# Kernel tuning notes

Hardware: AMD Instinct MI355X
Metric: run time of the kernel (lower is better)

Reference implementation:

```python
import jax, jax.numpy as jnp
import numpy as np

B, S, D_IN, D_OUT = 4, 2048, 4096, 4096
SPARSE_FRACTION = 0.9


def setup_inputs() -> dict:
    key = jax.random.key(0)
    k_x, k_w, k_m = jax.random.split(key, 3)
    x = jax.random.normal(k_x, (B, S, D_IN), dtype=jnp.float32)
    # kaiming_uniform_(a=sqrt(5)) -> U(-bound, bound), bound = sqrt(6/((1+a^2)*fan_in)) = 1/sqrt(fan_in)
    bound = 1.0 / np.sqrt(D_IN)
    weight = jax.random.uniform(k_w, (D_OUT, D_IN), dtype=jnp.float32,
                                minval=-bound, maxval=bound)
    # mask: exactly (1 - sparse_fraction) of entries are True (random permutation)
    num_params = D_OUT * D_IN
    num_sparse = int(num_params * SPARSE_FRACTION)
    perm = jax.random.permutation(k_m, num_params)
    mask_flat = jnp.ones((num_params,), dtype=jnp.float32).at[perm[:num_sparse]].set(0.0)
    mask = mask_flat.reshape(D_OUT, D_IN).astype(jnp.bool_)
    return {"x": x, "weight": weight, "mask": mask}


def reference(x, weight, mask):
    # masked_weight = weight * mask; out = x @ masked_weight.T
    masked_weight = weight * mask.astype(weight.dtype)  # [out, in]
    return jnp.einsum('bsi,oi->bso', x, masked_weight)
```

## Files before the change

### kernel.cpp

```cpp
#include <hip/hip_runtime.h>
#include <stdint.h>


static constexpr int Mdim = 8192;
static constexpr int Ndim = 4096;
static constexpr int Kdim = 4096;
static constexpr int BM = 128;
static constexpr int BN = 128;
static constexpr int BK = 64;

typedef __attribute__((ext_vector_type(8))) short short8;
typedef __attribute__((ext_vector_type(4))) float float4v;
typedef __attribute__((ext_vector_type(16))) float float16v;
typedef __attribute__((ext_vector_type(4))) int int4v;
typedef __attribute__((ext_vector_type(8))) unsigned short ushort8;

__device__ __forceinline__ unsigned short f32_to_bf16(float f) {
  union { float f; uint32_t u; } c; c.f = f;
  uint32_t u = c.u;
  u += 0x7fffu + ((u >> 16) & 1u);
  return (unsigned short)(u >> 16);
}

__global__ void detect_mask_kernel(const unsigned char* __restrict__ m, int* __restrict__ flag) {
  int found = 0;
  const int total = 1 << 20;
  for (int p = blockIdx.x * blockDim.x + threadIdx.x; p < total;
       p += gridDim.x * blockDim.x)
    found |= (m[4 * p + 1] != 0);
  if (__any(found) && (threadIdx.x & 63) == 0) atomicOr(flag, 1);
}

__global__ void cvt_x_kernel(const float* __restrict__ x, unsigned short* __restrict__ o) {
  long i = (blockIdx.x * (long)blockDim.x + threadIdx.x) * 8;
  float4v v0 = *(const float4v*)(x + i);
  float4v v1 = *(const float4v*)(x + i + 4);
  ushort8 r;
  r[0] = f32_to_bf16(v0[0]); r[1] = f32_to_bf16(v0[1]);
  r[2] = f32_to_bf16(v0[2]); r[3] = f32_to_bf16(v0[3]);
  r[4] = f32_to_bf16(v1[0]); r[5] = f32_to_bf16(v1[1]);
  r[6] = f32_to_bf16(v1[2]); r[7] = f32_to_bf16(v1[3]);
  *(ushort8*)(o + i) = r;
}

__global__ void cvt_w_kernel(const float* __restrict__ w, const unsigned char* __restrict__ mraw,
                             const int* __restrict__ flag, unsigned short* __restrict__ o) {
  long i = (blockIdx.x * (long)blockDim.x + threadIdx.x) * 8;
  float4v w0 = *(const float4v*)(w + i);
  float4v w1 = *(const float4v*)(w + i + 4);
  int m[8];
  if (*flag) {
    unsigned long long mb = *(const unsigned long long*)(mraw + i);
#pragma unroll
    for (int j = 0; j < 8; ++j) m[j] = ((mb >> (8 * j)) & 0xffull) != 0;
  } else {
    int4v a = *(const int4v*)((const int*)mraw + i);
    int4v b = *(const int4v*)((const int*)mraw + i + 4);
#pragma unroll
    for (int j = 0; j < 4; ++j) { m[j] = a[j] != 0; m[4 + j] = b[j] != 0; }
  }
  ushort8 r;
  r[0] = f32_to_bf16(m[0] ? w0[0] : 0.0f);
  r[1] = f32_to_bf16(m[1] ? w0[1] : 0.0f);
  r[2] = f32_to_bf16(m[2] ? w0[2] : 0.0f);
  r[3] = f32_to_bf16(m[3] ? w0[3] : 0.0f);
  r[4] = f32_to_bf16(m[4] ? w1[0] : 0.0f);
  r[5] = f32_to_bf16(m[5] ? w1[1] : 0.0f);
  r[6] = f32_to_bf16(m[6] ? w1[2] : 0.0f);
  r[7] = f32_to_bf16(m[7] ? w1[3] : 0.0f);
  *(ushort8*)(o + i) = r;
}

__global__ __launch_bounds__(256) void gemm_bt_kernel(const unsigned short* __restrict__ X,
                                                      const unsigned short* __restrict__ W,
                                                      float* __restrict__ O) {
  __shared__ short sA[BM * BK];
  __shared__ short sB[BN * BK];

  const int tid = threadIdx.x;
  const int lane = tid & 63;
  const int wave = tid >> 6;
  const int wr = wave >> 1;
  const int wc = wave & 1;

  const int bid = blockIdx.x;
  const int grp512 = bid >> 9;
  const int rres = bid & 511;
  const int tm = (grp512 << 4) | (rres & 15);
  const int tn = rres >> 4;
  const int row0 = tm * BM;
  const int col0 = tn * BN;

  float16v acc[2][2];
#pragma unroll
  for (int i = 0; i < 2; ++i)
#pragma unroll
    for (int j = 0; j < 2; ++j)
#pragma unroll
      for (int r = 0; r < 16; ++r) acc[i][j][r] = 0.f;

  int srow[4], scol[4];
#pragma unroll
  for (int r = 0; r < 4; ++r) {
    int c = r * 256 + tid;
    srow[r] = c >> 3;
    scol[r] = (((c & 7) ^ (srow[r] & 7)) * 8);
  }

  const int ml = lane & 31;
  const int kg = lane >> 5;
  const int sw = lane & 7;

  for (int kt = 0; kt < Kdim; kt += BK) {
#pragma unroll
    for (int r = 0; r < 4; ++r) {
      const unsigned short* gA = X + (long)(row0 + srow[r]) * Kdim + kt + scol[r];
      const unsigned short* gB = W + (long)(col0 + srow[r]) * Kdim + kt + scol[r];
      const int loff = (r * 256 + tid) * 16;
      __builtin_amdgcn_global_load_lds((const __attribute__((address_space(1))) void*)gA,
                                       (__attribute__((address_space(3))) void*)((char*)sA + loff),
                                       16, 0, 0);
      __builtin_amdgcn_global_load_lds((const __attribute__((address_space(1))) void*)gB,
                                       (__attribute__((address_space(3))) void*)((char*)sB + loff),
                                       16, 0, 0);
    }
    __syncthreads();

#pragma unroll
    for (int s = 0; s < 4; ++s) {
      const int pos = ((((s << 1) | kg) ^ sw) << 3);
      short8 a[2], b[2];
#pragma unroll
      for (int i = 0; i < 2; ++i)
        a[i] = *(const short8*)(sA + (wr * 64 + i * 32 + ml) * BK + pos);
#pragma unroll
      for (int j = 0; j < 2; ++j)
        b[j] = *(const short8*)(sB + (wc * 64 + j * 32 + ml) * BK + pos);
#pragma unroll
      for (int i = 0; i < 2; ++i)
#pragma unroll
        for (int j = 0; j < 2; ++j)
          acc[i][j] = __builtin_amdgcn_mfma_f32_32x32x16_bf16(a[i], b[j], acc[i][j], 0, 0, 0);
    }
    __syncthreads();
  }

#pragma unroll
  for (int i = 0; i < 2; ++i) {
#pragma unroll
    for (int j = 0; j < 2; ++j) {
      const long rbase = row0 + wr * 64 + i * 32;
      const long cg = col0 + wc * 64 + j * 32 + ml;
#pragma unroll
      for (int reg = 0; reg < 16; ++reg) {
        const long row = rbase + (reg & 3) + 8 * (reg >> 2) + 4 * kg;
        O[row * (long)Ndim + cg] = acc[i][j][reg];
      }
    }
  }
}

__global__ void gemm_fallback_kernel(const float* __restrict__ X, const float* __restrict__ Wt,
                                     const unsigned char* __restrict__ mraw,
                                     const int* __restrict__ flag, float* __restrict__ O) {
  __shared__ float sX[16][17];
  __shared__ float sW[16][17];
  const int tx = threadIdx.x & 15;
  const int ty = threadIdx.x >> 4;
  const long row = blockIdx.y * 16 + ty;
  const long colblock = blockIdx.x * 16;
  const int byteLayout = *flag;
  float acc = 0.f;
  for (int k0 = 0; k0 < Kdim; k0 += 16) {
    sX[ty][tx] = X[row * Kdim + k0 + tx];
    const long wi = (colblock + ty) * (long)Kdim + k0 + tx;
    const int mv = byteLayout ? (mraw[wi] != 0) : (((const int*)mraw)[wi] != 0);
    sW[ty][tx] = mv ? Wt[wi] : 0.f;
    __syncthreads();
#pragma unroll
    for (int k = 0; k < 16; ++k) acc += sX[ty][k] * sW[tx][k];
    __syncthreads();
  }
  O[row * Ndim + colblock + tx] = acc;
}

extern "C" void kernel_launch(void* const* d_in, const int* in_sizes, int n_in,
                              void* d_out, int out_size, void* d_ws, size_t ws_size,
                              hipStream_t stream) {
  const float* x = (const float*)d_in[0];
  const float* w = (const float*)d_in[1];
  const unsigned char* mask = (const unsigned char*)d_in[2];
  float* out = (float*)d_out;

  const size_t xb_off = 0;
  const size_t wb_off = (size_t)Mdim * Kdim * 2;
  const size_t flag_off = wb_off + (size_t)Ndim * Kdim * 2;
  const size_t needed = flag_off + 16;

  if (ws_size >= needed) {
    unsigned short* xb = (unsigned short*)((char*)d_ws + xb_off);
    unsigned short* wb = (unsigned short*)((char*)d_ws + wb_off);
    int* flag = (int*)((char*)d_ws + flag_off);

    hipMemsetAsync(flag, 0, sizeof(int), stream);
    detect_mask_kernel<<<64, 256, 0, stream>>>(mask, flag);
    cvt_x_kernel<<<(int)(((long)Mdim * Kdim / 8) / 256), 256, 0, stream>>>(x, xb);
    cvt_w_kernel<<<(int)(((long)Ndim * Kdim / 8) / 256), 256, 0, stream>>>(w, mask, flag, wb);
    gemm_bt_kernel<<<(Mdim / BM) * (Ndim / BN), 256, 0, stream>>>(xb, wb, out);
  } else {
    int* flag = (int*)d_ws;
    hipMemsetAsync(flag, 0, sizeof(int), stream);
    detect_mask_kernel<<<64, 256, 0, stream>>>(mask, flag);
    dim3 grid(Ndim / 16, Mdim / 16);
    gemm_fallback_kernel<<<grid, 256, 0, stream>>>(x, w, mask, flag, out);
  }
}
```

Before: 612.2 us.

## Store LDS tiles in MFMA fragment order, simplify tile mapping, widen conversion kernels

The GEMM now stages tiles into shared memory in the exact order each lane reads its MFMA fragment. This replaces the XOR-swizzled row layout and makes each lane's shared-memory read a contiguous 16-byte access. In exchange, each wave's global loads now cover only 32 bytes per row across 32 rows, where before 8 threads read 128 contiguous bytes of one row. The grouped block swizzle is replaced by plain row-major tile order, which may reduce L2 reuse. The conversion kernels handle 16 elements per thread instead of 8, and mask-layout detection is now a single block that samples a prefix and writes the flag directly, removing the memset launch.

```diff
diff --git a/kernel.cpp b/kernel.cpp
--- a/kernel.cpp
+++ b/kernel.cpp
@@ -13,6 +13,7 @@
 typedef __attribute__((ext_vector_type(4))) float float4v;
 typedef __attribute__((ext_vector_type(16))) float float16v;
 typedef __attribute__((ext_vector_type(4))) int int4v;
+typedef __attribute__((ext_vector_type(4))) unsigned int uint4v;
 typedef __attribute__((ext_vector_type(8))) unsigned short ushort8;
 
 __device__ __forceinline__ unsigned short f32_to_bf16(float f) {
@@ -23,52 +24,63 @@
 }
 
 __global__ void detect_mask_kernel(const unsigned char* __restrict__ m, int* __restrict__ flag) {
+  __shared__ int s;
+  if (threadIdx.x == 0) s = 0;
+  __syncthreads();
   int found = 0;
-  const int total = 1 << 20;
-  for (int p = blockIdx.x * blockDim.x + threadIdx.x; p < total;
-       p += gridDim.x * blockDim.x)
+  for (int p = threadIdx.x; p < 65536; p += blockDim.x)
     found |= (m[4 * p + 1] != 0);
-  if (__any(found) && (threadIdx.x & 63) == 0) atomicOr(flag, 1);
+  if (found) atomicOr(&s, 1);
+  __syncthreads();
+  if (threadIdx.x == 0) *flag = s;
 }
 
 __global__ void cvt_x_kernel(const float* __restrict__ x, unsigned short* __restrict__ o) {
-  long i = (blockIdx.x * (long)blockDim.x + threadIdx.x) * 8;
-  float4v v0 = *(const float4v*)(x + i);
-  float4v v1 = *(const float4v*)(x + i + 4);
-  ushort8 r;
-  r[0] = f32_to_bf16(v0[0]); r[1] = f32_to_bf16(v0[1]);
-  r[2] = f32_to_bf16(v0[2]); r[3] = f32_to_bf16(v0[3]);
-  r[4] = f32_to_bf16(v1[0]); r[5] = f32_to_bf16(v1[1]);
-  r[6] = f32_to_bf16(v1[2]); r[7] = f32_to_bf16(v1[3]);
-  *(ushort8*)(o + i) = r;
+  long i = (blockIdx.x * (long)blockDim.x + threadIdx.x) * 16;
+  float4v v[4];
+#pragma unroll
+  for (int t = 0; t < 4; ++t) v[t] = *(const float4v*)(x + i + 4 * t);
+  ushort8 r0, r1;
+#pragma unroll
+  for (int t = 0; t < 4; ++t) r0[t] = f32_to_bf16(v[0][t]);
+#pragma unroll
+  for (int t = 0; t < 4; ++t) r0[4 + t] = f32_to_bf16(v[1][t]);
+#pragma unroll
+  for (int t = 0; t < 4; ++t) r1[t] = f32_to_bf16(v[2][t]);
+#pragma unroll
+  for (int t = 0; t < 4; ++t) r1[4 + t] = f32_to_bf16(v[3][t]);
+  *(ushort8*)(o + i) = r0;
+  *(ushort8*)(o + i + 8) = r1;
 }
 
 __global__ void cvt_w_kernel(const float* __restrict__ w, const unsigned char* __restrict__ mraw,
                              const int* __restrict__ flag, unsigned short* __restrict__ o) {
-  long i = (blockIdx.x * (long)blockDim.x + threadIdx.x) * 8;
-  float4v w0 = *(const float4v*)(w + i);
-  float4v w1 = *(const float4v*)(w + i + 4);
-  int m[8];
+  long i = (blockIdx.x * (long)blockDim.x + threadIdx.x) * 16;
+  float4v v[4];
+#pragma unroll
+  for (int t = 0; t < 4; ++t) v[t] = *(const float4v*)(w + i + 4 * t);
+  int m[16];
   if (*flag) {
-    unsigned long long mb = *(const unsigned long long*)(mraw + i);
-#pragma unroll
-    for (int j = 0; j < 8; ++j) m[j] = ((mb >> (8 * j)) & 0xffull) != 0;
+    uint4v mb = *(const uint4v*)(mraw + i);
+#pragma unroll
+    for (int t = 0; t < 4; ++t)
+#pragma unroll
+      for (int j = 0; j < 4; ++j) m[4 * t + j] = ((mb[t] >> (8 * j)) & 0xffu) != 0;
   } else {
-    int4v a = *(const int4v*)((const int*)mraw + i);
-    int4v b = *(const int4v*)((const int*)mraw + i + 4);
-#pragma unroll
-    for (int j = 0; j < 4; ++j) { m[j] = a[j] != 0; m[4 + j] = b[j] != 0; }
-  }
-  ushort8 r;
-  r[0] = f32_to_bf16(m[0] ? w0[0] : 0.0f);
-  r[1] = f32_to_bf16(m[1] ? w0[1] : 0.0f);
-  r[2] = f32_to_bf16(m[2] ? w0[2] : 0.0f);
-  r[3] = f32_to_bf16(m[3] ? w0[3] : 0.0f);
-  r[4] = f32_to_bf16(m[4] ? w1[0] : 0.0f);
-  r[5] = f32_to_bf16(m[5] ? w1[1] : 0.0f);
-  r[6] = f32_to_bf16(m[6] ? w1[2] : 0.0f);
-  r[7] = f32_to_bf16(m[7] ? w1[3] : 0.0f);
-  *(ushort8*)(o + i) = r;
+#pragma unroll
+    for (int t = 0; t < 4; ++t) {
+      int4v mv = *(const int4v*)((const int*)mraw + i + 4 * t);
+#pragma unroll
+      for (int j = 0; j < 4; ++j) m[4 * t + j] = mv[j] != 0;
+    }
+  }
+  ushort8 r0, r1;
+#pragma unroll
+  for (int t = 0; t < 8; ++t) r0[t] = f32_to_bf16(m[t] ? v[t >> 2][t & 3] : 0.0f);
+#pragma unroll
+  for (int t = 0; t < 8; ++t) r1[t] = f32_to_bf16(m[8 + t] ? v[2 + (t >> 2)][t & 3] : 0.0f);
+  *(ushort8*)(o + i) = r0;
+  *(ushort8*)(o + i + 8) = r1;
 }
 
 __global__ __launch_bounds__(256) void gemm_bt_kernel(const unsigned short* __restrict__ X,
@@ -83,11 +95,8 @@
   const int wr = wave >> 1;
   const int wc = wave & 1;
 
-  const int bid = blockIdx.x;
-  const int grp512 = bid >> 9;
-  const int rres = bid & 511;
-  const int tm = (grp512 << 4) | (rres & 15);
-  const int tn = rres >> 4;
+  const int tm = blockIdx.x >> 5;
+  const int tn = blockIdx.x & 31;
   const int row0 = tm * BM;
   const int col0 = tn * BN;
 
@@ -99,23 +108,20 @@
 #pragma unroll
       for (int r = 0; r < 16; ++r) acc[i][j][r] = 0.f;
 
-  int srow[4], scol[4];
-#pragma unroll
-  for (int r = 0; r < 4; ++r) {
-    int c = r * 256 + tid;
-    srow[r] = c >> 3;
-    scol[r] = (((c & 7) ^ (srow[r] & 7)) * 8);
-  }
+  const int st_row = tid & 31;
+  const int st_col = (tid >> 5) * 8;
 
   const int ml = lane & 31;
   const int kg = lane >> 5;
-  const int sw = lane & 7;
+
+  const short* aBase = sA + lane * 8;
+  const short* bBase = sB + lane * 8;
 
   for (int kt = 0; kt < Kdim; kt += BK) {
 #pragma unroll
     for (int r = 0; r < 4; ++r) {
-      const unsigned short* gA = X + (long)(row0 + srow[r]) * Kdim + kt + scol[r];
-      const unsigned short* gB = W + (long)(col0 + srow[r]) * Kdim + kt + scol[r];
+      const unsigned short* gA = X + (long)(row0 + r * 32 + st_row) * Kdim + kt + st_col;
+      const unsigned short* gB = W + (long)(col0 + r * 32 + st_row) * Kdim + kt + st_col;
       const int loff = (r * 256 + tid) * 16;
       __builtin_amdgcn_global_load_lds((const __attribute__((address_space(1))) void*)gA,
                                        (__attribute__((address_space(3))) void*)((char*)sA + loff),
@@ -128,14 +134,13 @@
 
 #pragma unroll
     for (int s = 0; s < 4; ++s) {
-      const int pos = ((((s << 1) | kg) ^ sw) << 3);
       short8 a[2], b[2];
 #pragma unroll
       for (int i = 0; i < 2; ++i)
-        a[i] = *(const short8*)(sA + (wr * 64 + i * 32 + ml) * BK + pos);
+        a[i] = *(const short8*)(aBase + (wr * 2 + i) * 2048 + s * 512);
 #pragma unroll
       for (int j = 0; j < 2; ++j)
-        b[j] = *(const short8*)(sB + (wc * 64 + j * 32 + ml) * BK + pos);
+        b[j] = *(const short8*)(bBase + (wc * 2 + j) * 2048 + s * 512);
 #pragma unroll
       for (int i = 0; i < 2; ++i)
 #pragma unroll
@@ -202,15 +207,13 @@
     unsigned short* wb = (unsigned short*)((char*)d_ws + wb_off);
     int* flag = (int*)((char*)d_ws + flag_off);
 
-    hipMemsetAsync(flag, 0, sizeof(int), stream);
-    detect_mask_kernel<<<64, 256, 0, stream>>>(mask, flag);
-    cvt_x_kernel<<<(int)(((long)Mdim * Kdim / 8) / 256), 256, 0, stream>>>(x, xb);
-    cvt_w_kernel<<<(int)(((long)Ndim * Kdim / 8) / 256), 256, 0, stream>>>(w, mask, flag, wb);
+    detect_mask_kernel<<<1, 1024, 0, stream>>>(mask, flag);
+    cvt_x_kernel<<<(int)(((long)Mdim * Kdim / 16) / 256), 256, 0, stream>>>(x, xb);
+    cvt_w_kernel<<<(int)(((long)Ndim * Kdim / 16) / 256), 256, 0, stream>>>(w, mask, flag, wb);
     gemm_bt_kernel<<<(Mdim / BM) * (Ndim / BN), 256, 0, stream>>>(xb, wb, out);
   } else {
     int* flag = (int*)d_ws;
-    hipMemsetAsync(flag, 0, sizeof(int), stream);
-    detect_mask_kernel<<<64, 256, 0, stream>>>(mask, flag);
+    detect_mask_kernel<<<1, 1024, 0, stream>>>(mask, flag);
     dim3 grid(Ndim / 16, Mdim / 16);
     gemm_fallback_kernel<<<grid, 256, 0, stream>>>(x, w, mask, flag, out);
   }
```

New measurement: 796.4 us. 30.1% more time.
